# Optimization experiments

Measured on AMD Instinct MI355X. Metric: run time of the kernel, lower is better.

Reference implementation:

```python
import jax, jax.numpy as jnp
import numpy as np


def setup_inputs() -> dict:
    key = jax.random.key(0)
    ks = jax.random.split(key, 8)
    E = 2_000_000          # num facts (edges)
    B, M = 8, 2000         # batch, max_local_entity -> B*M = 16000 entity slots
    R, D = 2000, 128       # num relations, hidden size (in_features == out_features)
    return {
        "local_entity": jax.random.randint(ks[0], (B, M), 0, M),
        "batch_heads": jax.random.randint(ks[1], (E,), 0, B * M),
        "batch_tails": jax.random.randint(ks[2], (E,), 0, B * M),
        "batch_rels": jax.random.randint(ks[3], (E,), 0, R),
        "val_one": jax.random.uniform(ks[4], (E,), dtype=jnp.float32),
        "rel_features": jax.random.normal(ks[5], (R, D), dtype=jnp.float32),
        "W": jax.random.normal(ks[6], (D, D), dtype=jnp.float32) * 0.05,
        "b": jax.random.normal(ks[7], (D,), dtype=jnp.float32) * 0.05,
    }


def reference(local_entity, batch_heads, batch_tails, batch_rels, val_one,
              rel_features, W, b):
    B, M = local_entity.shape
    num_ent = B * M
    # gather relation features per fact, linear transform (nn.Linear: x @ W.T + b)
    fact_rel = rel_features[batch_rels]            # [E, D]
    fact_val = fact_rel @ W.T + b                  # [E, D]
    # sparse COO mm == weighted scatter-add of fact_val into entity slots
    weighted = fact_val * val_one[:, None]         # [E, D]
    tail_agg = jax.ops.segment_sum(weighted, batch_tails, num_segments=num_ent)
    head_agg = jax.ops.segment_sum(weighted, batch_heads, num_segments=num_ent)
    f2e_emb = jax.nn.relu(tail_agg + head_agg)     # [B*M, D]
    return f2e_emb.reshape(B, M, -1)
```

## Files before the change

### kernel.cpp

```cpp
#include <hip/hip_runtime.h>
#include <hip/hip_bf16.h>
#include <cstdint>

typedef _Float16 half2v __attribute__((ext_vector_type(2)));

#define EPB   16
#define MAXNB 1024
#define FPB   8192
#define FPT   16
#define SORTCAP 4608
#define CPT   9


__device__ __forceinline__ float pay_val(unsigned p) {
    return (float)__builtin_bit_cast(_Float16, (unsigned short)(p & 0xFFFFu));
}

__global__ void rwb_row_kernel(const float* __restrict__ rel, const float* __restrict__ W,
                               const float* __restrict__ b, _Float16* __restrict__ rwb,
                               int R) {
    const int k = blockIdx.x;
    const int n = threadIdx.x;
    __shared__ float relk[128];
    relk[n] = rel[(size_t)k * 128 + n];
    __syncthreads();
    const float4* w4 = reinterpret_cast<const float4*>(W + (size_t)n * 128);
    const float4* r4 = reinterpret_cast<const float4*>(relk);
    float acc = 0.f;
#pragma unroll
    for (int i = 0; i < 32; ++i) {
        float4 a = r4[i], w = w4[i];
        acc += a.x * w.x + a.y * w.y + a.z * w.z + a.w * w.w;
    }
    rwb[(size_t)k * 128 + n] = (_Float16)(acc + b[n]);
}

__device__ __noinline__ void spill_add(float* __restrict__ out, const _Float16* __restrict__ rwb,
                                       int v, unsigned pay) {
    const int r = (int)((pay >> 16) & 0xFFFu);
    const float val = pay_val(pay);
    float* o = out + (size_t)v * 128;
    const _Float16* rw = rwb + (size_t)r * 128;
    for (int n = 0; n < 128; ++n) unsafeAtomicAdd(o + n, val * (float)rw[n]);
}

__global__ __launch_bounds__(512) void bin_kernel(
    const int* __restrict__ heads, const int* __restrict__ tails,
    const int* __restrict__ rels, const float* __restrict__ val,
    int* __restrict__ gcnt, unsigned* __restrict__ slots,
    const _Float16* __restrict__ rwb, float* __restrict__ out,
    int E, int NB, int CAPB) {
    __shared__ int cnt[MAXNB];
    __shared__ int gbase[MAXNB];
    const int t = threadIdx.x;
    for (int k = t; k < NB; k += 512) cnt[k] = 0;
    __syncthreads();

    const int base = blockIdx.x * FPB;
    unsigned payT[FPT], payH[FPT], prT[FPT], prH[FPT];
#pragma unroll
    for (int u = 0; u < FPT; ++u) {
        const int i = base + u * 512 + t;
        prT[u] = 0xFFFFFFFFu;
        prH[u] = 0xFFFFFFFFu;
        if (i < E) {
            const int tl = tails[i], hd = heads[i], r = rels[i];
            const unsigned hv =
                (unsigned)__builtin_bit_cast(unsigned short, (_Float16)val[i]);
            const int bt = tl >> 4, bh = hd >> 4;
            payT[u] = ((unsigned)(tl & 15) << 28) | ((unsigned)r << 16) | hv;
            payH[u] = ((unsigned)(hd & 15) << 28) | ((unsigned)r << 16) | hv;
            const int rt = atomicAdd(&cnt[bt], 1);
            const int rh = atomicAdd(&cnt[bh], 1);
            prT[u] = ((unsigned)bt << 16) | (unsigned)rt;
            prH[u] = ((unsigned)bh << 16) | (unsigned)rh;
        }
    }
    __syncthreads();
    for (int k = t; k < NB; k += 512) {
        const int c = cnt[k];
        gbase[k] = c ? atomicAdd(&gcnt[k], c) : 0;
    }
    __syncthreads();
#pragma unroll
    for (int u = 0; u < FPT; ++u) {
        if (prT[u] != 0xFFFFFFFFu) {
            {
                const int b1 = (int)(prT[u] >> 16);
                const int pos = gbase[b1] + (int)(prT[u] & 0xFFFFu);
                if (pos < CAPB) slots[(size_t)b1 * CAPB + pos] = payT[u];
                else spill_add(out, rwb, (b1 << 4) | (int)(payT[u] >> 28), payT[u]);
            }
            {
                const int b1 = (int)(prH[u] >> 16);
                const int pos = gbase[b1] + (int)(prH[u] & 0xFFFFu);
                if (pos < CAPB) slots[(size_t)b1 * CAPB + pos] = payH[u];
                else spill_add(out, rwb, (b1 << 4) | (int)(payH[u] >> 28), payH[u]);
            }
        }
    }
}

__global__ __launch_bounds__(512) void gather_kernel(
    const unsigned* __restrict__ slots, const int* __restrict__ gcnt,
    const _Float16* __restrict__ rwb, float* __restrict__ out,
    int NUMENT, int CAPB) {
    __shared__ unsigned se[SORTCAP];
    __shared__ int cnt[EPB], basep[EPB];
    const int t = threadIdx.x;
    const int b = blockIdx.x;
    if (t < EPB) cnt[t] = 0;
    __syncthreads();

    int deg = gcnt[b];
    if (deg > CAPB) deg = CAPB;
    const unsigned* sl = slots + (size_t)b * CAPB;

    unsigned e[CPT];
    int rk[CPT];
#pragma unroll
    for (int u = 0; u < CPT; ++u) {
        const int k = t + u * 512;
        rk[u] = -1;
        if (k < deg) {
            e[u] = sl[k];
            rk[u] = atomicAdd(&cnt[(int)(e[u] >> 28)], 1);
        }
    }
    __syncthreads();
    if (t == 0) {
        int s = 0;
#pragma unroll
        for (int i = 0; i < EPB; ++i) { basep[i] = s; s += cnt[i]; }
    }
    __syncthreads();
#pragma unroll
    for (int u = 0; u < CPT; ++u)
        if (rk[u] >= 0) se[basep[(int)(e[u] >> 28)] + rk[u]] = e[u];
    __syncthreads();

    const int wv = t >> 6, lane = t & 63;
    const int loff = lane * 2;
#pragma unroll
    for (int ei = 0; ei < 2; ++ei) {
        const int le = wv * 2 + ei;
        const int vent = b * EPB + le;
        const int s0 = basep[le], c = cnt[le];
        float a0 = 0.f, a1 = 0.f;
        int j = 0;
        for (; j + 8 <= c; j += 8) {
            unsigned q[8];
#pragma unroll
            for (int u = 0; u < 8; ++u) q[u] = se[s0 + j + u];
            unsigned qs[8];
#pragma unroll
            for (int u = 0; u < 8; ++u) qs[u] = __builtin_amdgcn_readfirstlane(q[u]);
            unsigned rw[8];
#pragma unroll
            for (int u = 0; u < 8; ++u) {
                const _Float16* rowp = rwb + (size_t)((qs[u] >> 16) & 0xFFFu) * 128;
                rw[u] = *reinterpret_cast<const unsigned*>(rowp + loff);
            }
#pragma unroll
            for (int u = 0; u < 8; ++u) {
                const float w = (float)__builtin_bit_cast(
                    _Float16, (unsigned short)(qs[u] & 0xFFFFu));
                const half2v h = __builtin_bit_cast(half2v, rw[u]);
                a0 = fmaf(w, (float)h[0], a0);
                a1 = fmaf(w, (float)h[1], a1);
            }
        }
        for (; j < c; ++j) {
            const unsigned q = se[s0 + j];
            const unsigned qs = __builtin_amdgcn_readfirstlane(q);
            const _Float16* rowp = rwb + (size_t)((qs >> 16) & 0xFFFu) * 128;
            const unsigned rwv = *reinterpret_cast<const unsigned*>(rowp + loff);
            const float w = (float)__builtin_bit_cast(
                _Float16, (unsigned short)(qs & 0xFFFFu));
            const half2v h = __builtin_bit_cast(half2v, rwv);
            a0 = fmaf(w, (float)h[0], a0);
            a1 = fmaf(w, (float)h[1], a1);
        }
        if (vent < NUMENT) {
            float* op = out + (size_t)vent * 128 + loff;
            float2 sp = *reinterpret_cast<const float2*>(op);
            float2 o;
            o.x = fmaxf(a0 + sp.x, 0.f);
            o.y = fmaxf(a1 + sp.y, 0.f);
            *reinterpret_cast<float2*>(op) = o;
        }
    }
}

__global__ void rwb_f32_kernel(const float* __restrict__ rel, const float* __restrict__ W,
                               const float* __restrict__ b, float* __restrict__ rwb, int R) {
    const int k = blockIdx.x;
    const int n = threadIdx.x;
    __shared__ float relk[128];
    relk[n] = rel[(size_t)k * 128 + n];
    __syncthreads();
    const float4* w4 = reinterpret_cast<const float4*>(W + (size_t)n * 128);
    const float4* r4 = reinterpret_cast<const float4*>(relk);
    float acc = 0.f;
#pragma unroll
    for (int i = 0; i < 32; ++i) {
        float4 a = r4[i], w = w4[i];
        acc += a.x * w.x + a.y * w.y + a.z * w.z + a.w * w.w;
    }
    rwb[(size_t)k * 128 + n] = acc + b[n];
}

__global__ void scatter_vec_kernel(const int* __restrict__ heads, const int* __restrict__ tails,
                                   const int* __restrict__ rels, const float* __restrict__ val,
                                   const float* __restrict__ rwb, float* __restrict__ out,
                                   long long nitems) {
    const long long i = (long long)blockIdx.x * blockDim.x + threadIdx.x;
    if (i >= nitems) return;
    const int e = (int)(i >> 5);
    const int c = (int)(i & 31) * 4;
    const float v = val[e];
    float4 rw = *reinterpret_cast<const float4*>(rwb + (size_t)rels[e] * 128 + c);
    float* pt = out + (size_t)tails[e] * 128 + c;
    float* ph = out + (size_t)heads[e] * 128 + c;
    unsafeAtomicAdd(pt + 0, v * rw.x); unsafeAtomicAdd(pt + 1, v * rw.y);
    unsafeAtomicAdd(pt + 2, v * rw.z); unsafeAtomicAdd(pt + 3, v * rw.w);
    unsafeAtomicAdd(ph + 0, v * rw.x); unsafeAtomicAdd(ph + 1, v * rw.y);
    unsafeAtomicAdd(ph + 2, v * rw.z); unsafeAtomicAdd(ph + 3, v * rw.w);
}

__global__ void relu_kernel(float* __restrict__ out, int n4) {
    const int i = blockIdx.x * blockDim.x + threadIdx.x;
    if (i >= n4) return;
    float4* p = reinterpret_cast<float4*>(out) + i;
    float4 v = *p;
    v.x = fmaxf(v.x, 0.f); v.y = fmaxf(v.y, 0.f);
    v.z = fmaxf(v.z, 0.f); v.w = fmaxf(v.w, 0.f);
    *p = v;
}

extern "C" void kernel_launch(void* const* d_in, const int* in_sizes, int n_in,
                              void* d_out, int out_size, void* d_ws, size_t ws_size,
                              hipStream_t stream) {
    const int* heads = (const int*)d_in[1];
    const int* tails = (const int*)d_in[2];
    const int* rels  = (const int*)d_in[3];
    const float* val  = (const float*)d_in[4];
    const float* relf = (const float*)d_in[5];
    const float* W    = (const float*)d_in[6];
    const float* b    = (const float*)d_in[7];
    float* out = (float*)d_out;

    const int NUMENT = in_sizes[0];
    const int E      = in_sizes[1];
    const int D      = in_sizes[7];
    const int R      = in_sizes[5] / D;

    const int NB = (NUMENT + EPB - 1) / EPB;
    const long long mean = (2LL * E * EPB) / (NUMENT > 0 ? NUMENT : 1);
    int CAPB = (int)(mean + mean / 16 + 256);

    const size_t rwb_bytes = (size_t)R * D * sizeof(_Float16);
    const size_t off_gcnt  = (rwb_bytes + 255) & ~(size_t)255;
    const size_t gcnt_b    = (size_t)NB * sizeof(int);
    const size_t off_slots = (off_gcnt + gcnt_b + 255) & ~(size_t)255;
    const size_t slots_b   = (size_t)NB * CAPB * sizeof(unsigned);

    if (NB <= MAXNB && R < 4096 && CAPB <= SORTCAP &&
        ws_size >= off_slots + slots_b) {
        _Float16* rwb   = (_Float16*)d_ws;
        int* gcnt       = (int*)((char*)d_ws + off_gcnt);
        unsigned* slots = (unsigned*)((char*)d_ws + off_slots);

        hipMemsetAsync(gcnt, 0, gcnt_b, stream);
        hipMemsetAsync(out, 0, (size_t)out_size * sizeof(float), stream);
        rwb_row_kernel<<<R, 128, 0, stream>>>(relf, W, b, rwb, R);
        bin_kernel<<<(E + FPB - 1) / FPB, 512, 0, stream>>>(
            heads, tails, rels, val, gcnt, slots, rwb, out, E, NB, CAPB);
        gather_kernel<<<NB, 512, 0, stream>>>(slots, gcnt, rwb, out, NUMENT, CAPB);
    } else {
        float* rwb = (float*)d_ws;
        hipMemsetAsync(out, 0, (size_t)out_size * sizeof(float), stream);
        rwb_f32_kernel<<<R, 128, 0, stream>>>(relf, W, b, rwb, R);
        const long long items = (long long)E * 32;
        scatter_vec_kernel<<<(unsigned)((items + 255) / 256), 256, 0, stream>>>(
            heads, tails, rels, val, rwb, out, items);
        relu_kernel<<<(out_size / 4 + 255) / 256, 256, 0, stream>>>(out, out_size / 4);
    }
}
```

Baseline: 205.5 us.

## Fuse memsets into rwb kernel, widen bin blocks, use fma_mix in gather

Zeroing of the bucket counters and the output buffer moves into the relation-transform kernel, which removes two memset launches. The binning kernel now runs 1024-thread blocks with 8 facts per thread instead of 512 threads with 16, which lowers register pressure per thread. The gather inner loop uses inline v_fma_mix_f32 asm so the fp16 weight and fp16 row values are multiplied and accumulated in fp32 without separate conversions. Relying on inline asm with SGPR operand constraints carries a risk of miscompilation or register-allocation trouble.

```diff
diff --git a/kernel.cpp b/kernel.cpp
--- a/kernel.cpp
+++ b/kernel.cpp
@@ -7,7 +7,7 @@
 #define EPB   16
 #define MAXNB 1024
 #define FPB   8192
-#define FPT   16
+#define FPT   8
 #define SORTCAP 4608
 #define CPT   9
 
@@ -18,9 +18,18 @@
 
 __global__ void rwb_row_kernel(const float* __restrict__ rel, const float* __restrict__ W,
                                const float* __restrict__ b, _Float16* __restrict__ rwb,
-                               int R) {
+                               int R, int* __restrict__ gcnt, float* __restrict__ out,
+                               int NB, int NUMENT) {
     const int k = blockIdx.x;
     const int n = threadIdx.x;
+    const int gtid = k * 128 + n;
+    const int gstr = gridDim.x * 128;
+    for (int i = gtid; i < NB; i += gstr) gcnt[i] = 0;
+    const int n4 = NUMENT * 32;
+    const float4 z = {0.f, 0.f, 0.f, 0.f};
+    for (int i = gtid; i < n4; i += gstr)
+        reinterpret_cast<float4*>(out)[i] = z;
+
     __shared__ float relk[128];
     relk[n] = rel[(size_t)k * 128 + n];
     __syncthreads();
@@ -44,7 +53,7 @@
     for (int n = 0; n < 128; ++n) unsafeAtomicAdd(o + n, val * (float)rw[n]);
 }
 
-__global__ __launch_bounds__(512) void bin_kernel(
+__global__ __launch_bounds__(1024) void bin_kernel(
     const int* __restrict__ heads, const int* __restrict__ tails,
     const int* __restrict__ rels, const float* __restrict__ val,
     int* __restrict__ gcnt, unsigned* __restrict__ slots,
@@ -53,14 +62,14 @@
     __shared__ int cnt[MAXNB];
     __shared__ int gbase[MAXNB];
     const int t = threadIdx.x;
-    for (int k = t; k < NB; k += 512) cnt[k] = 0;
+    for (int k = t; k < NB; k += 1024) cnt[k] = 0;
     __syncthreads();
 
     const int base = blockIdx.x * FPB;
     unsigned payT[FPT], payH[FPT], prT[FPT], prH[FPT];
 #pragma unroll
     for (int u = 0; u < FPT; ++u) {
-        const int i = base + u * 512 + t;
+        const int i = base + u * 1024 + t;
         prT[u] = 0xFFFFFFFFu;
         prH[u] = 0xFFFFFFFFu;
         if (i < E) {
@@ -77,7 +86,7 @@
         }
     }
     __syncthreads();
-    for (int k = t; k < NB; k += 512) {
+    for (int k = t; k < NB; k += 1024) {
         const int c = cnt[k];
         gbase[k] = c ? atomicAdd(&gcnt[k], c) : 0;
     }
@@ -163,11 +172,10 @@
             }
 #pragma unroll
             for (int u = 0; u < 8; ++u) {
-                const float w = (float)__builtin_bit_cast(
-                    _Float16, (unsigned short)(qs[u] & 0xFFFFu));
-                const half2v h = __builtin_bit_cast(half2v, rw[u]);
-                a0 = fmaf(w, (float)h[0], a0);
-                a1 = fmaf(w, (float)h[1], a1);
+                asm("v_fma_mix_f32 %[d], %[s0], %[s1], %[d] op_sel:[0,0,0] op_sel_hi:[1,1,0]"
+                    : [d]"+v"(a0) : [s0]"s"(qs[u]), [s1]"v"(rw[u]));
+                asm("v_fma_mix_f32 %[d], %[s0], %[s1], %[d] op_sel:[0,1,0] op_sel_hi:[1,1,0]"
+                    : [d]"+v"(a1) : [s0]"s"(qs[u]), [s1]"v"(rw[u]));
             }
         }
         for (; j < c; ++j) {
@@ -175,11 +183,10 @@
             const unsigned qs = __builtin_amdgcn_readfirstlane(q);
             const _Float16* rowp = rwb + (size_t)((qs >> 16) & 0xFFFu) * 128;
             const unsigned rwv = *reinterpret_cast<const unsigned*>(rowp + loff);
-            const float w = (float)__builtin_bit_cast(
-                _Float16, (unsigned short)(qs & 0xFFFFu));
-            const half2v h = __builtin_bit_cast(half2v, rwv);
-            a0 = fmaf(w, (float)h[0], a0);
-            a1 = fmaf(w, (float)h[1], a1);
+            asm("v_fma_mix_f32 %[d], %[s0], %[s1], %[d] op_sel:[0,0,0] op_sel_hi:[1,1,0]"
+                : [d]"+v"(a0) : [s0]"s"(qs), [s1]"v"(rwv));
+            asm("v_fma_mix_f32 %[d], %[s0], %[s1], %[d] op_sel:[0,1,0] op_sel_hi:[1,1,0]"
+                : [d]"+v"(a1) : [s0]"s"(qs), [s1]"v"(rwv));
         }
         if (vent < NUMENT) {
             float* op = out + (size_t)vent * 128 + loff;
@@ -271,10 +278,8 @@
         int* gcnt       = (int*)((char*)d_ws + off_gcnt);
         unsigned* slots = (unsigned*)((char*)d_ws + off_slots);
 
-        hipMemsetAsync(gcnt, 0, gcnt_b, stream);
-        hipMemsetAsync(out, 0, (size_t)out_size * sizeof(float), stream);
-        rwb_row_kernel<<<R, 128, 0, stream>>>(relf, W, b, rwb, R);
-        bin_kernel<<<(E + FPB - 1) / FPB, 512, 0, stream>>>(
+        rwb_row_kernel<<<R, 128, 0, stream>>>(relf, W, b, rwb, R, gcnt, out, NB, NUMENT);
+        bin_kernel<<<(E + FPB - 1) / FPB, 1024, 0, stream>>>(
             heads, tails, rels, val, gcnt, slots, rwb, out, E, NB, CAPB);
         gather_kernel<<<NB, 512, 0, stream>>>(slots, gcnt, rwb, out, NUMENT, CAPB);
     } else {
```

Measured after the change: 196.3 us. 1.05x faster.
